# Optimization experiments

Measured on AMD Instinct MI355X. Metric: run time of the kernel, lower is better.

## Reference

```python
import jax, jax.numpy as jnp
import numpy as np

B, S, D, H = 2, 2048, 512, 8
HD = D // H
SPARSITY = 0.15
KTOP = max(1, int(S * SPARSITY))          # 307 important rows
HALF_WIN = min(32, S // 4) // 2           # 16 -> window |i-j| <= 16
RC = min(16, S // 8)                      # 16 random links per query token


def setup_inputs() -> dict:
    key = jax.random.key(0)
    ks = jax.random.split(key, 8)
    s = 0.02
    return {
        "x":  jax.random.normal(ks[0], (B, S, D), jnp.float32),
        "Wq": jax.random.normal(ks[1], (D, D), jnp.float32) * s,
        "bq": jnp.zeros((D,), jnp.float32),
        "Wk": jax.random.normal(ks[2], (D, D), jnp.float32) * s,
        "bk": jnp.zeros((D,), jnp.float32),
        "Wv": jax.random.normal(ks[3], (D, D), jnp.float32) * s,
        "bv": jnp.zeros((D,), jnp.float32),
        "Wo": jax.random.normal(ks[4], (D, D), jnp.float32) * s,
        "bo": jnp.zeros((D,), jnp.float32),
        "Ws1": jax.random.normal(ks[5], (D, D // 2), jnp.float32) * s,
        "bs1": jnp.zeros((D // 2,), jnp.float32),
        "Ws2": jax.random.normal(ks[6], (D // 2, 1), jnp.float32) * s,
        "bs2": jnp.zeros((1,), jnp.float32),
        # models torch.randperm(S)[:RC] per (b, i); duplicates are harmless for set-to-1
        "rand_idx": jax.random.randint(ks[7], (B, S, RC), 0, S, jnp.int32),
    }


def _sparse_mask(x, Ws1, bs1, Ws2, bs2, rand_idx):
    # importance scorer: Linear -> ReLU -> Linear -> Sigmoid, squeeze(-1)
    imp = jax.nn.sigmoid(jax.nn.relu(x @ Ws1 + bs1) @ Ws2 + bs2)[..., 0]  # [B,S]
    _, top_idx = jax.lax.top_k(imp, KTOP)                                  # [B,KTOP]
    brange = jnp.arange(B)
    row_imp = jnp.zeros((B, S), bool).at[brange[:, None], top_idx].set(True)
    idx = jnp.arange(S)
    win = jnp.abs(idx[:, None] - idx[None, :]) <= HALF_WIN                 # [S,S]
    rmask = jnp.zeros((B, S, S), bool).at[
        brange[:, None, None], idx[None, :, None], rand_idx].set(True)    # [B,S,S]
    mask = row_imp[:, :, None] | win[None, :, :] | rmask                   # [B,S,S]
    tril = idx[:, None] >= idx[None, :]                                    # causal (mask * (causal==0))
    return mask & tril


def reference(x, Wq, bq, Wk, bk, Wv, bv, Wo, bo, Ws1, bs1, Ws2, bs2, rand_idx):
    allowed = _sparse_mask(x, Ws1, bs1, Ws2, bs2, rand_idx)                # [B,S,S] bool
    q = (x @ Wq + bq).reshape(B, S, H, HD).transpose(0, 2, 1, 3)           # [B,H,S,HD]
    k = (x @ Wk + bk).reshape(B, S, H, HD).transpose(0, 2, 1, 3)
    v = (x @ Wv + bv).reshape(B, S, H, HD).transpose(0, 2, 1, 3)
    scores = jnp.einsum('bhid,bhjd->bhij', q, k) / jnp.sqrt(jnp.float32(HD))
    scores = jnp.where(allowed[:, None, :, :], scores, -jnp.inf)
    attn = jax.nn.softmax(scores, axis=-1)                                 # every row has j=i allowed
    out = jnp.einsum('bhij,bhjd->bhid', attn, v)
    out = out.transpose(0, 2, 1, 3).reshape(B, S, D)
    return out @ Wo + bo
```

## Files before the change

kernel.cpp:

```cpp
#include <hip/hip_runtime.h>
#include <math.h>

typedef unsigned short u16;
typedef unsigned int u32;
typedef unsigned long long u64;
typedef short bf16x8 __attribute__((ext_vector_type(8)));
typedef float f32x4 __attribute__((ext_vector_type(4)));

constexpr int NB = 2, NS = 2048, ND = 512, NH = 8, NHD = 64;
constexpr int NKTOP = 307, NHWIN = 16, NRC = 16;
constexpr int NILIST = 320;
constexpr int NSPAR = NS - NKTOP;
constexpr int NSPAD = 1744;
constexpr int NCHUNK = 8;
constexpr int LDSPAD = 40;
constexpr int LDSK64 = 72;
constexpr int PSTR = 72;

__device__ __forceinline__ u16 f2bf(float f) {
  u32 u = __builtin_bit_cast(u32, f);
  u32 r = (u + 0x7FFFu + ((u >> 16) & 1u)) >> 16;
  return (u16)r;
}
__device__ __forceinline__ float bf2f(short v) {
  return __builtin_bit_cast(float, (u32)(u16)v << 16);
}

__global__ __launch_bounds__(256) void csa_cvt_w(const float* __restrict__ W0, const float* __restrict__ W1,
                                                 const float* __restrict__ W2, const float* __restrict__ W3,
                                                 u16* __restrict__ wt) {
  __shared__ float tile[64][33];
  int w = blockIdx.z;
  const float* src = (w == 0) ? W0 : (w == 1) ? W1 : (w == 2) ? W2 : W3;
  int kb = blockIdx.x * 64, nb = blockIdx.y * 32;
  int tx = threadIdx.x & 31, ty = threadIdx.x >> 5;
  for (int i = ty; i < 64; i += 8) tile[i][tx] = src[(size_t)(kb + i) * ND + nb + tx];
  __syncthreads();
  u16* dst = wt + (size_t)w * ND * ND;
  for (int n = ty; n < 32; n += 8) {
    u32 pk = (u32)f2bf(tile[2 * tx][n]) | ((u32)f2bf(tile[2 * tx + 1][n]) << 16);
    *(u32*)(&dst[(size_t)(nb + n) * ND + kb + 2 * tx]) = pk;
  }
}

__global__ __launch_bounds__(256) void csa_scorer(const float* __restrict__ x, const float* __restrict__ Ws1,
                                                  const float* __restrict__ bs1, const float* __restrict__ Ws2,
                                                  float* __restrict__ part) {
  __shared__ float As[32][68];
  __shared__ float Bs[32][68];
  const int tid = threadIdx.x;
  const int m0 = blockIdx.x * 64, n0 = blockIdx.y * 64;
  const int ty = tid >> 4, tx = tid & 15;
  float acc[4][4] = {};
  const int arow = tid & 63, aks = (tid >> 6) * 8;
  const int bk = tid >> 3, bc = (tid & 7) * 8;
  for (int k0 = 0; k0 < ND; k0 += 32) {
    __syncthreads();
    {
      float4 a0 = *(const float4*)(&x[(size_t)(m0 + arow) * ND + k0 + aks]);
      float4 a1 = *(const float4*)(&x[(size_t)(m0 + arow) * ND + k0 + aks + 4]);
      As[aks + 0][arow] = a0.x; As[aks + 1][arow] = a0.y;
      As[aks + 2][arow] = a0.z; As[aks + 3][arow] = a0.w;
      As[aks + 4][arow] = a1.x; As[aks + 5][arow] = a1.y;
      As[aks + 6][arow] = a1.z; As[aks + 7][arow] = a1.w;
    }
    *(float4*)(&Bs[bk][bc]) = *(const float4*)(&Ws1[(size_t)(k0 + bk) * 256 + n0 + bc]);
    *(float4*)(&Bs[bk][bc + 4]) = *(const float4*)(&Ws1[(size_t)(k0 + bk) * 256 + n0 + bc + 4]);
    __syncthreads();
    for (int k = 0; k < 32; k++) {
      float4 av = *(const float4*)(&As[k][ty * 4]);
      float4 bv = *(const float4*)(&Bs[k][tx * 4]);
      float aa[4] = {av.x, av.y, av.z, av.w};
      float bb[4] = {bv.x, bv.y, bv.z, bv.w};
      for (int i = 0; i < 4; i++)
        for (int j = 0; j < 4; j++)
          acc[i][j] += aa[i] * bb[j];
    }
  }
  float4 w2 = *(const float4*)(&Ws2[n0 + tx * 4]);
  float4 b1 = *(const float4*)(&bs1[n0 + tx * 4]);
  for (int i = 0; i < 4; i++) {
    float p = fmaxf(acc[i][0] + b1.x, 0.f) * w2.x + fmaxf(acc[i][1] + b1.y, 0.f) * w2.y +
              fmaxf(acc[i][2] + b1.z, 0.f) * w2.z + fmaxf(acc[i][3] + b1.w, 0.f) * w2.w;
    for (int off = 1; off < 16; off <<= 1) p += __shfl_xor(p, off, 64);
    if (tx == 0) part[(size_t)(m0 + ty * 4 + i) * 4 + blockIdx.y] = p;
  }
}

__global__ __launch_bounds__(256) void csa_rank(const float* __restrict__ part, int* __restrict__ rowimp) {
  __shared__ float vals[NS];
  const int b = blockIdx.y;
  {
    int t8 = threadIdx.x * 8;
    for (int e = 0; e < 8; e++) {
      float4 pp = *(const float4*)(&part[(size_t)(b * NS + t8 + e) * 4]);
      vals[t8 + e] = (pp.x + pp.y) + (pp.z + pp.w);
    }
  }
  __syncthreads();
  const int wave = threadIdx.x >> 6, lane = threadIdx.x & 63;
  const int s0 = blockIdx.x * 8 + wave * 2;
  const int s1 = s0 + 1;
  const float v0 = vals[s0], v1 = vals[s1];
  int r0 = 0, r1 = 0;
  for (int t = lane; t < NS; t += 64) {
    float u = vals[t];
    r0 += (int)((u > v0) | ((u == v0) & (t < s0)));
    r1 += (int)((u > v1) | ((u == v1) & (t < s1)));
  }
  for (int off = 1; off < 64; off <<= 1) {
    r0 += __shfl_xor(r0, off, 64);
    r1 += __shfl_xor(r1, off, 64);
  }
  if (lane == 0) {
    rowimp[b * NS + s0] = (r0 < NKTOP) ? 1 : 0;
    rowimp[b * NS + s1] = (r1 < NKTOP) ? 1 : 0;
  }
}

__global__ __launch_bounds__(256) void csa_ilist(const int* __restrict__ rowimp, int* __restrict__ ilist,
                                                 int* __restrict__ nlist) {
  __shared__ int cs[256];
  int b = blockIdx.x, t = threadIdx.x;
  int flags[8], sum = 0;
  for (int k = 0; k < 8; k++) {
    flags[k] = rowimp[b * NS + t * 8 + k];
    sum += flags[k];
  }
  cs[t] = sum;
  __syncthreads();
  for (int off = 1; off < 256; off <<= 1) {
    int v = (t >= off) ? cs[t - off] : 0;
    __syncthreads();
    cs[t] += v;
    __syncthreads();
  }
  int pos = cs[t] - sum;
  for (int k = 0; k < 8; k++) {
    int r = t * 8 + k;
    if (flags[k]) ilist[b * NILIST + pos++] = r;
    else nlist[b * NSPAD + (r - pos)] = r;
  }
  if (t < NILIST - NKTOP) ilist[b * NILIST + NKTOP + t] = -1;
  if (t < NSPAD - NSPAR) nlist[b * NSPAD + NSPAR + t] = -1;
}

__global__ __launch_bounds__(256) void csa_gemm_qkv(const float* __restrict__ x, const u16* __restrict__ Bt,
                                                    const float* __restrict__ bq, const float* __restrict__ bk,
                                                    const float* __restrict__ bv, u16* __restrict__ qb,
                                                    u16* __restrict__ kb, u16* __restrict__ vtb,
                                                    u16* __restrict__ vb) {
  __shared__ __attribute__((aligned(16))) u16 As[128 * LDSPAD];
  __shared__ __attribute__((aligned(16))) u16 Bs[64 * LDSPAD];
  const int tid = threadIdx.x;
  const int wave = tid >> 6, lane = tid & 63;
  const int quad = lane >> 4, col = lane & 15;
  const int m0 = blockIdx.x * 128;
  const int n0 = blockIdx.y * 64;
  const f32x4 zf = {0.f, 0.f, 0.f, 0.f};
  f32x4 acc[2][4] = {{zf, zf, zf, zf}, {zf, zf, zf, zf}};
  const int sar = tid >> 1, sak = (tid & 1) * 16;
  const int sbr = tid >> 2, sbk = (tid & 3) * 8;
  for (int k0 = 0; k0 < ND; k0 += 32) {
    __syncthreads();
    {
      const float* xp = &x[(size_t)(m0 + sar) * ND + k0 + sak];
      float4 v0 = *(const float4*)(xp), v1 = *(const float4*)(xp + 4);
      float4 v2 = *(const float4*)(xp + 8), v3 = *(const float4*)(xp + 12);
      u32 w0 = (u32)f2bf(v0.x) | ((u32)f2bf(v0.y) << 16);
      u32 w1 = (u32)f2bf(v0.z) | ((u32)f2bf(v0.w) << 16);
      u32 w2 = (u32)f2bf(v1.x) | ((u32)f2bf(v1.y) << 16);
      u32 w3 = (u32)f2bf(v1.z) | ((u32)f2bf(v1.w) << 16);
      u32 w4 = (u32)f2bf(v2.x) | ((u32)f2bf(v2.y) << 16);
      u32 w5 = (u32)f2bf(v2.z) | ((u32)f2bf(v2.w) << 16);
      u32 w6 = (u32)f2bf(v3.x) | ((u32)f2bf(v3.y) << 16);
      u32 w7 = (u32)f2bf(v3.z) | ((u32)f2bf(v3.w) << 16);
      u32* ap = (u32*)&As[sar * LDSPAD + sak];
      ap[0] = w0; ap[1] = w1; ap[2] = w2; ap[3] = w3;
      ap[4] = w4; ap[5] = w5; ap[6] = w6; ap[7] = w7;
    }
    *(uint4*)(&Bs[sbr * LDSPAD + sbk]) = *(const uint4*)(&Bt[(size_t)(n0 + sbr) * ND + k0 + sbk]);
    __syncthreads();
    bf16x8 af0 = *(const bf16x8*)(&As[(wave * 32 + col) * LDSPAD + quad * 8]);
    bf16x8 af1 = *(const bf16x8*)(&As[(wave * 32 + 16 + col) * LDSPAD + quad * 8]);
    for (int c = 0; c < 4; c++) {
      bf16x8 bfr = *(const bf16x8*)(&Bs[(c * 16 + col) * LDSPAD + quad * 8]);
      acc[0][c] = __builtin_amdgcn_mfma_f32_16x16x32_bf16(af0, bfr, acc[0][c], 0, 0, 0);
      acc[1][c] = __builtin_amdgcn_mfma_f32_16x16x32_bf16(af1, bfr, acc[1][c], 0, 0, 0);
    }
  }
  const int w = n0 >> 9;
  const float* bias = (w == 0) ? bq : (w == 1) ? bk : bv;
  for (int c = 0; c < 4; c++) {
    const int ng = n0 + c * 16 + col;
    const int nn = ng & 511, hh = nn >> 6, hd = nn & 63;
    const float bvv = bias[nn];
    for (int r = 0; r < 2; r++) {
      for (int rr = 0; rr < 4; rr++) {
        const int m = m0 + wave * 32 + r * 16 + quad * 4 + rr;
        const int bb = m >> 11, s = m & (NS - 1);
        u16 v16 = f2bf(acc[r][c][rr] + bvv);
        if (w == 0) qb[((size_t)(bb * NH + hh) * NS + s) * NHD + hd] = v16;
        else if (w == 1) kb[((size_t)(bb * NH + hh) * NS + s) * NHD + hd] = v16;
        else {
          vtb[((size_t)(bb * NH + hh) * NHD + hd) * NS + s] = v16;
          vb[((size_t)(bb * NH + hh) * NS + s) * NHD + hd] = v16;
        }
      }
    }
  }
}

__global__ __launch_bounds__(256) void csa_gemm_out(const u16* __restrict__ A, const u16* __restrict__ Bt,
                                                    const float* __restrict__ bias, float* __restrict__ outp) {
  __shared__ __attribute__((aligned(16))) u16 As[64 * LDSK64];
  __shared__ __attribute__((aligned(16))) u16 Bs[64 * LDSK64];
  const int tid = threadIdx.x;
  const int wave = tid >> 6, lane = tid & 63;
  const int quad = lane >> 4, col = lane & 15;
  const int m0 = blockIdx.x * 64;
  const int n0 = blockIdx.y * 64;
  const f32x4 zf = {0.f, 0.f, 0.f, 0.f};
  f32x4 acc[4] = {zf, zf, zf, zf};
  const int sr = tid >> 2, sk = (tid & 3) * 16;
  for (int k0 = 0; k0 < ND; k0 += 64) {
    __syncthreads();
    *(uint4*)(&As[sr * LDSK64 + sk]) = *(const uint4*)(&A[(size_t)(m0 + sr) * ND + k0 + sk]);
    *(uint4*)(&As[sr * LDSK64 + sk + 8]) = *(const uint4*)(&A[(size_t)(m0 + sr) * ND + k0 + sk + 8]);
    *(uint4*)(&Bs[sr * LDSK64 + sk]) = *(const uint4*)(&Bt[(size_t)(n0 + sr) * ND + k0 + sk]);
    *(uint4*)(&Bs[sr * LDSK64 + sk + 8]) = *(const uint4*)(&Bt[(size_t)(n0 + sr) * ND + k0 + sk + 8]);
    __syncthreads();
    bf16x8 af0 = *(const bf16x8*)(&As[(wave * 16 + col) * LDSK64 + quad * 8]);
    bf16x8 af1 = *(const bf16x8*)(&As[(wave * 16 + col) * LDSK64 + 32 + quad * 8]);
    for (int nt = 0; nt < 4; nt++) {
      bf16x8 bf0 = *(const bf16x8*)(&Bs[(nt * 16 + col) * LDSK64 + quad * 8]);
      bf16x8 bf1 = *(const bf16x8*)(&Bs[(nt * 16 + col) * LDSK64 + 32 + quad * 8]);
      acc[nt] = __builtin_amdgcn_mfma_f32_16x16x32_bf16(af0, bf0, acc[nt], 0, 0, 0);
      acc[nt] = __builtin_amdgcn_mfma_f32_16x16x32_bf16(af1, bf1, acc[nt], 0, 0, 0);
    }
  }
  for (int nt = 0; nt < 4; nt++) {
    const int n = n0 + nt * 16 + col;
    const float bvv = bias[n];
    for (int r = 0; r < 4; r++) {
      const int m = m0 + wave * 16 + quad * 4 + r;
      outp[(size_t)m * ND + n] = acc[nt][r] + bvv;
    }
  }
}

__global__ __launch_bounds__(64) void csa_attn_imp(const u16* __restrict__ qb, const u16* __restrict__ kb,
                                                   const u16* __restrict__ vtb, const int* __restrict__ ilist,
                                                   float* __restrict__ pbuf) {
  const int lane = threadIdx.x;
  const int quad = lane >> 4, col = lane & 15;
  const int qt = blockIdx.x;
  const int chunk = blockIdx.y;
  const int bh = blockIdx.z;
  const int b = bh >> 3, h = bh & 7;

  const int* il = ilist + b * NILIST;
  const u16* qptr = qb + (size_t)(b * NH + h) * NS * NHD;
  const u16* kptr = kb + (size_t)(b * NH + h) * NS * NHD;
  const u16* vptr = vtb + (size_t)(b * NH + h) * NHD * NS;

  const int iq = il[qt * 16 + col];
  const int qrow = (iq < 0) ? 0 : iq;
  bf16x8 qf0 = *(const bf16x8*)(qptr + qrow * NHD + quad * 8);
  bf16x8 qf1 = *(const bf16x8*)(qptr + qrow * NHD + 32 + quad * 8);

  const f32x4 zf = {0.f, 0.f, 0.f, 0.f};
  float m_r[4], l_r[4];
  f32x4 of[4];
  int irow[4];
  for (int r = 0; r < 4; r++) {
    m_r[r] = -INFINITY;
    l_r[r] = 0.f;
    irow[r] = il[qt * 16 + quad * 4 + r];
  }
  for (int n = 0; n < 4; n++) of[n] = zf;

  __shared__ __attribute__((aligned(16))) u16 Pl[16 * PSTR];

  const int max_i = il[(qt * 16 + 15 > NKTOP - 1) ? (NKTOP - 1) : (qt * 16 + 15)];
  const int ntiles = (max_i >> 6) + 1;
  for (int t = chunk; t < ntiles; t += NCHUNK) {
    const int j0 = t * 64;
    f32x4 cg[4];
    for (int g = 0; g < 4; g++) {
      const int jb = j0 + g * 16;
      bf16x8 k0f = *(const bf16x8*)(kptr + (jb + col) * NHD + quad * 8);
      bf16x8 k1f = *(const bf16x8*)(kptr + (jb + col) * NHD + 32 + quad * 8);
      f32x4 c = zf;
      c = __builtin_amdgcn_mfma_f32_16x16x32_bf16(qf0, k0f, c, 0, 0, 0);
      c = __builtin_amdgcn_mfma_f32_16x16x32_bf16(qf1, k1f, c, 0, 0, 0);
      cg[g] = c;
    }
    float ps[4][4], alpha[4];
    for (int r = 0; r < 4; r++) {
      const int i = irow[r];
      float s[4];
      float vmax = -INFINITY;
      for (int g = 0; g < 4; g++) {
        s[g] = (j0 + g * 16 + col <= i) ? cg[g][r] * 0.125f : -INFINITY;
        vmax = fmaxf(vmax, s[g]);
      }
      for (int off = 1; off < 16; off <<= 1) vmax = fmaxf(vmax, __shfl_xor(vmax, off, 64));
      float newm = fmaxf(m_r[r], vmax);
      bool dead = (newm == -INFINITY);
      float a = dead ? 1.f : __expf(m_r[r] - newm);
      float psum = 0.f;
      for (int g = 0; g < 4; g++) {
        float p = dead ? 0.f : __expf(s[g] - newm);
        ps[r][g] = p;
        psum += p;
      }
      for (int off = 1; off < 16; off <<= 1) psum += __shfl_xor(psum, off, 64);
      m_r[r] = newm;
      l_r[r] = l_r[r] * a + psum;
      alpha[r] = a;
    }
    for (int n = 0; n < 4; n++)
      for (int r = 0; r < 4; r++) of[n][r] *= alpha[r];
    __syncthreads();
    for (int r = 0; r < 4; r++)
      for (int g = 0; g < 4; g++)
        Pl[(quad * 4 + r) * PSTR + g * 16 + col] = f2bf(ps[r][g]);
    __syncthreads();
    bf16x8 pf0 = *(const bf16x8*)(&Pl[col * PSTR + quad * 8]);
    bf16x8 pf1 = *(const bf16x8*)(&Pl[col * PSTR + 32 + quad * 8]);
    for (int vn = 0; vn < 4; vn++) {
      bf16x8 vf0 = *(const bf16x8*)(vptr + (size_t)(vn * 16 + col) * NS + j0 + quad * 8);
      bf16x8 vf1 = *(const bf16x8*)(vptr + (size_t)(vn * 16 + col) * NS + j0 + 32 + quad * 8);
      of[vn] = __builtin_amdgcn_mfma_f32_16x16x32_bf16(pf0, vf0, of[vn], 0, 0, 0);
      of[vn] = __builtin_amdgcn_mfma_f32_16x16x32_bf16(pf1, vf1, of[vn], 0, 0, 0);
    }
  }
  float* pr = pbuf + ((size_t)(bh * NCHUNK + chunk) * NILIST + qt * 16) * 66;
  for (int r = 0; r < 4; r++) {
    const int row = quad * 4 + r;
    if (col == 0) {
      pr[row * 66 + 0] = m_r[r];
      pr[row * 66 + 1] = l_r[r];
    }
    for (int vn = 0; vn < 4; vn++)
      pr[row * 66 + 2 + vn * 16 + col] = of[vn][r];
  }
}

__global__ __launch_bounds__(64) void csa_merge(const float* __restrict__ pbuf, const int* __restrict__ ilist,
                                                u16* __restrict__ attnb) {
  const int kp = blockIdx.x, h = blockIdx.y, b = blockIdx.z;
  const int lane = threadIdx.x;
  const int z = b * NH + h;
  float mc[NCHUNK], lc[NCHUNK], mstar = -INFINITY;
  for (int c = 0; c < NCHUNK; c++) {
    const float* base = pbuf + ((size_t)(z * NCHUNK + c) * NILIST + kp) * 66;
    mc[c] = base[0];
    lc[c] = base[1];
    mstar = fmaxf(mstar, mc[c]);
  }
  float lsum = 0.f, osum = 0.f;
  for (int c = 0; c < NCHUNK; c++) {
    const float* base = pbuf + ((size_t)(z * NCHUNK + c) * NILIST + kp) * 66;
    float w = (mc[c] == -INFINITY) ? 0.f : __expf(mc[c] - mstar);
    lsum += w * lc[c];
    osum += w * base[2 + lane];
  }
  const int i = ilist[b * NILIST + kp];
  attnb[((size_t)(b * NS + i) * NH + h) * NHD + lane] = f2bf(osum / lsum);
}

__global__ __launch_bounds__(256) void csa_attn_sparse(const u16* __restrict__ qb, const u16* __restrict__ kb,
                                                       const u16* __restrict__ vb, const int* __restrict__ nlist,
                                                       const int* __restrict__ rand_idx, u16* __restrict__ attnb) {
  __shared__ __attribute__((aligned(16))) u16 ql[4][64];
  __shared__ float pl[4][33];
  __shared__ int jl[4][33];
  const int wave = threadIdx.x >> 6, lane = threadIdx.x & 63;
  const int slot = blockIdx.x * 4 + wave;
  const int h = blockIdx.y, b = blockIdx.z;
  const int i = nlist[b * NSPAD + slot];
  const int iv = (i < 0) ? 0 : i;

  const u16* qrow = qb + ((size_t)(b * NH + h) * NS + iv) * NHD;
  const u16* kbase = kb + (size_t)(b * NH + h) * NS * NHD;
  const u16* vbase = vb + (size_t)(b * NH + h) * NS * NHD;

  if (lane < 8) *(bf16x8*)(&ql[wave][lane * 8]) = *(const bf16x8*)(qrow + lane * 8);
  __syncthreads();

  float sd = bf2f((short)ql[wave][lane]) * bf2f((short)kbase[(size_t)iv * NHD + lane]);
  for (int off = 1; off < 64; off <<= 1) sd += __shfl_xor(sd, off, 64);
  sd *= 0.125f;

  const int c = lane >> 1, half = lane & 1;
  int j, valid;
  if (c < 16) {
    j = i - NHWIN + c;
    valid = (j >= 0);
  } else {
    const int* rr = rand_idx + ((size_t)b * NS + iv) * NRC;
    const int cr = c - 16;
    j = rr[cr];
    valid = (j <= i - NHWIN - 1);
    for (int cp = 0; cp < cr; cp++) valid &= (rr[cp] != j);
  }
  const int jr = valid ? j : 0;
  float s = 0.f;
  {
    const u16* krow = kbase + (size_t)jr * NHD + half * 32;
    for (int c8 = 0; c8 < 4; c8++) {
      bf16x8 kv = *(const bf16x8*)(krow + c8 * 8);
      bf16x8 qv = *(const bf16x8*)(&ql[wave][half * 32 + c8 * 8]);
      for (int e = 0; e < 8; e++) s += bf2f(qv[e]) * bf2f(kv[e]);
    }
  }
  s += __shfl_xor(s, 1, 64);
  s = valid ? s * 0.125f : -INFINITY;

  float smax = s;
  for (int off = 1; off < 64; off <<= 1) smax = fmaxf(smax, __shfl_xor(smax, off, 64));
  smax = fmaxf(smax, sd);
  float p = valid ? __expf(s - smax) : 0.f;
  float pd = __expf(sd - smax);
  float pm = (half == 0) ? p : 0.f;
  for (int off = 1; off < 64; off <<= 1) pm += __shfl_xor(pm, off, 64);
  const float lsum = pm + pd;

  if (half == 0) {
    pl[wave][c] = p;
    jl[wave][c] = jr;
  }
  if (lane == 0) {
    pl[wave][32] = pd;
    jl[wave][32] = iv;
  }
  __syncthreads();

  float o = 0.f;
  for (int jj = 0; jj < 33; jj++) {
    const int jk = __builtin_amdgcn_readfirstlane(jl[wave][jj]);
    const float pj = pl[wave][jj];
    o += pj * bf2f((short)vbase[(size_t)jk * NHD + lane]);
  }
  if (i >= 0)
    attnb[((size_t)(b * NS + i) * NH + h) * NHD + lane] = f2bf(o / lsum);
}

extern "C" void kernel_launch(void* const* d_in, const int* in_sizes, int n_in,
                              void* d_out, int out_size, void* d_ws, size_t ws_size,
                              hipStream_t stream) {
  const float* x = (const float*)d_in[0];
  const float* bq = (const float*)d_in[2];
  const float* bk = (const float*)d_in[4];
  const float* bv = (const float*)d_in[6];
  const float* bo = (const float*)d_in[8];
  const float* Ws1 = (const float*)d_in[9];
  const float* bs1 = (const float*)d_in[10];
  const float* Ws2 = (const float*)d_in[11];
  const int* rand_idx = (const int*)d_in[13];
  float* out = (float*)d_out;

  char* p = (char*)d_ws;
  u16* wt = (u16*)p;         p += (size_t)4 * ND * ND * 2;
  u16* qbuf = (u16*)p;       p += (size_t)NB * NH * NS * NHD * 2;
  u16* kbuf = (u16*)p;       p += (size_t)NB * NH * NS * NHD * 2;
  u16* vtbuf = (u16*)p;      p += (size_t)NB * NH * NHD * NS * 2;
  u16* vbuf = (u16*)p;       p += (size_t)NB * NH * NS * NHD * 2;
  u16* attnb = (u16*)p;      p += (size_t)NB * NS * ND * 2;
  float* part = (float*)p;   p += (size_t)NB * NS * 4 * 4;
  int* rowimp = (int*)p;     p += (size_t)NB * NS * 4;
  int* ilist = (int*)p;      p += (size_t)NB * NILIST * 4;
  int* nlist = (int*)p;      p += (size_t)NB * NSPAD * 4;
  float* pbuf = (float*)p;

  csa_cvt_w<<<dim3(8, 16, 4), 256, 0, stream>>>((const float*)d_in[1], (const float*)d_in[3],
                                                (const float*)d_in[5], (const float*)d_in[7], wt);

  csa_scorer<<<dim3(NB * NS / 64, 4), 256, 0, stream>>>(x, Ws1, bs1, Ws2, part);
  csa_rank<<<dim3(NS / 8, NB), 256, 0, stream>>>(part, rowimp);
  csa_ilist<<<dim3(NB), 256, 0, stream>>>(rowimp, ilist, nlist);

  csa_gemm_qkv<<<dim3(32, 24), 256, 0, stream>>>(x, wt, bq, bk, bv, qbuf, kbuf, vtbuf, vbuf);

  csa_attn_imp<<<dim3(NILIST / 16, NCHUNK, NB * NH), 64, 0, stream>>>(qbuf, kbuf, vtbuf, ilist, pbuf);
  csa_attn_sparse<<<dim3(NSPAD / 4, NH, NB), 256, 0, stream>>>(qbuf, kbuf, vbuf, nlist, rand_idx, attnb);
  csa_merge<<<dim3(NKTOP, NH, NB), 64, 0, stream>>>(pbuf, ilist, attnb);

  csa_gemm_out<<<dim3(64, 8), 256, 0, stream>>>(attnb, wt + 3 * (size_t)ND * ND, bo, out);
}
```

Before: 209.5 us.

## Merge weight-convert/scorer and sparse/important attention kernels; use wave-local LDS fences

After: 217.7 us. +3.9%, slower.

```diff
diff --git a/kernel.cpp b/kernel.cpp
--- a/kernel.cpp
+++ b/kernel.cpp
@@ -16,6 +16,8 @@
 constexpr int LDSPAD = 40;
 constexpr int LDSK64 = 72;
 constexpr int PSTR = 72;
+constexpr int NSBLK = (NSPAD / 4) * NH * NB;
+constexpr int NIBLK = (NILIST / 16) * NCHUNK * (NB * NH) / 4;
 
 __device__ __forceinline__ u16 f2bf(float f) {
   u32 u = __builtin_bit_cast(u32, f);
@@ -25,65 +27,72 @@
 __device__ __forceinline__ float bf2f(short v) {
   return __builtin_bit_cast(float, (u32)(u16)v << 16);
 }
-
-__global__ __launch_bounds__(256) void csa_cvt_w(const float* __restrict__ W0, const float* __restrict__ W1,
-                                                 const float* __restrict__ W2, const float* __restrict__ W3,
-                                                 u16* __restrict__ wt) {
-  __shared__ float tile[64][33];
-  int w = blockIdx.z;
-  const float* src = (w == 0) ? W0 : (w == 1) ? W1 : (w == 2) ? W2 : W3;
-  int kb = blockIdx.x * 64, nb = blockIdx.y * 32;
-  int tx = threadIdx.x & 31, ty = threadIdx.x >> 5;
-  for (int i = ty; i < 64; i += 8) tile[i][tx] = src[(size_t)(kb + i) * ND + nb + tx];
-  __syncthreads();
-  u16* dst = wt + (size_t)w * ND * ND;
-  for (int n = ty; n < 32; n += 8) {
-    u32 pk = (u32)f2bf(tile[2 * tx][n]) | ((u32)f2bf(tile[2 * tx + 1][n]) << 16);
-    *(u32*)(&dst[(size_t)(nb + n) * ND + kb + 2 * tx]) = pk;
-  }
-}
-
-__global__ __launch_bounds__(256) void csa_scorer(const float* __restrict__ x, const float* __restrict__ Ws1,
-                                                  const float* __restrict__ bs1, const float* __restrict__ Ws2,
-                                                  float* __restrict__ part) {
-  __shared__ float As[32][68];
-  __shared__ float Bs[32][68];
+__device__ __forceinline__ void wave_lds_fence() {
+  __builtin_amdgcn_s_waitcnt(0xC07F);
+  __builtin_amdgcn_wave_barrier();
+}
+
+__global__ __launch_bounds__(256) void csa_prep(const float* __restrict__ W0, const float* __restrict__ W1,
+                                                const float* __restrict__ W2, const float* __restrict__ W3,
+                                                u16* __restrict__ wt, const float* __restrict__ x,
+                                                const float* __restrict__ Ws1, const float* __restrict__ bs1,
+                                                const float* __restrict__ Ws2, float* __restrict__ part) {
+  __shared__ float sh[2 * 32 * 68];
   const int tid = threadIdx.x;
-  const int m0 = blockIdx.x * 64, n0 = blockIdx.y * 64;
-  const int ty = tid >> 4, tx = tid & 15;
-  float acc[4][4] = {};
-  const int arow = tid & 63, aks = (tid >> 6) * 8;
-  const int bk = tid >> 3, bc = (tid & 7) * 8;
-  for (int k0 = 0; k0 < ND; k0 += 32) {
-    __syncthreads();
-    {
-      float4 a0 = *(const float4*)(&x[(size_t)(m0 + arow) * ND + k0 + aks]);
-      float4 a1 = *(const float4*)(&x[(size_t)(m0 + arow) * ND + k0 + aks + 4]);
-      As[aks + 0][arow] = a0.x; As[aks + 1][arow] = a0.y;
-      As[aks + 2][arow] = a0.z; As[aks + 3][arow] = a0.w;
-      As[aks + 4][arow] = a1.x; As[aks + 5][arow] = a1.y;
-      As[aks + 6][arow] = a1.z; As[aks + 7][arow] = a1.w;
-    }
-    *(float4*)(&Bs[bk][bc]) = *(const float4*)(&Ws1[(size_t)(k0 + bk) * 256 + n0 + bc]);
-    *(float4*)(&Bs[bk][bc + 4]) = *(const float4*)(&Ws1[(size_t)(k0 + bk) * 256 + n0 + bc + 4]);
-    __syncthreads();
-    for (int k = 0; k < 32; k++) {
-      float4 av = *(const float4*)(&As[k][ty * 4]);
-      float4 bv = *(const float4*)(&Bs[k][tx * 4]);
-      float aa[4] = {av.x, av.y, av.z, av.w};
-      float bb[4] = {bv.x, bv.y, bv.z, bv.w};
-      for (int i = 0; i < 4; i++)
-        for (int j = 0; j < 4; j++)
-          acc[i][j] += aa[i] * bb[j];
-    }
-  }
-  float4 w2 = *(const float4*)(&Ws2[n0 + tx * 4]);
-  float4 b1 = *(const float4*)(&bs1[n0 + tx * 4]);
-  for (int i = 0; i < 4; i++) {
-    float p = fmaxf(acc[i][0] + b1.x, 0.f) * w2.x + fmaxf(acc[i][1] + b1.y, 0.f) * w2.y +
-              fmaxf(acc[i][2] + b1.z, 0.f) * w2.z + fmaxf(acc[i][3] + b1.w, 0.f) * w2.w;
-    for (int off = 1; off < 16; off <<= 1) p += __shfl_xor(p, off, 64);
-    if (tx == 0) part[(size_t)(m0 + ty * 4 + i) * 4 + blockIdx.y] = p;
+  if (blockIdx.x < 256) {
+    const int m0 = (blockIdx.x & 63) * 64, n0 = (blockIdx.x >> 6) * 64;
+    float(*As)[68] = (float(*)[68])sh;
+    float(*Bs)[68] = (float(*)[68])(sh + 32 * 68);
+    const int ty = tid >> 4, tx = tid & 15;
+    float acc[4][4] = {};
+    const int arow = tid & 63, aks = (tid >> 6) * 8;
+    const int bk = tid >> 3, bc = (tid & 7) * 8;
+    for (int k0 = 0; k0 < ND; k0 += 32) {
+      __syncthreads();
+      {
+        float4 a0 = *(const float4*)(&x[(size_t)(m0 + arow) * ND + k0 + aks]);
+        float4 a1 = *(const float4*)(&x[(size_t)(m0 + arow) * ND + k0 + aks + 4]);
+        As[aks + 0][arow] = a0.x; As[aks + 1][arow] = a0.y;
+        As[aks + 2][arow] = a0.z; As[aks + 3][arow] = a0.w;
+        As[aks + 4][arow] = a1.x; As[aks + 5][arow] = a1.y;
+        As[aks + 6][arow] = a1.z; As[aks + 7][arow] = a1.w;
+      }
+      *(float4*)(&Bs[bk][bc]) = *(const float4*)(&Ws1[(size_t)(k0 + bk) * 256 + n0 + bc]);
+      *(float4*)(&Bs[bk][bc + 4]) = *(const float4*)(&Ws1[(size_t)(k0 + bk) * 256 + n0 + bc + 4]);
+      __syncthreads();
+      for (int k = 0; k < 32; k++) {
+        float4 av = *(const float4*)(&As[k][ty * 4]);
+        float4 bv = *(const float4*)(&Bs[k][tx * 4]);
+        float aa[4] = {av.x, av.y, av.z, av.w};
+        float bb[4] = {bv.x, bv.y, bv.z, bv.w};
+        for (int i = 0; i < 4; i++)
+          for (int j = 0; j < 4; j++)
+            acc[i][j] += aa[i] * bb[j];
+      }
+    }
+    float4 w2 = *(const float4*)(&Ws2[n0 + tx * 4]);
+    float4 b1 = *(const float4*)(&bs1[n0 + tx * 4]);
+    for (int i = 0; i < 4; i++) {
+      float p = fmaxf(acc[i][0] + b1.x, 0.f) * w2.x + fmaxf(acc[i][1] + b1.y, 0.f) * w2.y +
+                fmaxf(acc[i][2] + b1.z, 0.f) * w2.z + fmaxf(acc[i][3] + b1.w, 0.f) * w2.w;
+      for (int off = 1; off < 16; off <<= 1) p += __shfl_xor(p, off, 64);
+      if (tx == 0) part[(size_t)(m0 + ty * 4 + i) * 4 + (blockIdx.x >> 6)] = p;
+    }
+  } else {
+    const int cb = blockIdx.x - 256;
+    const int w = cb >> 7;
+    const int kb = ((cb & 127) >> 4) * 64;
+    const int nb = (cb & 15) * 32;
+    const float* src = (w == 0) ? W0 : (w == 1) ? W1 : (w == 2) ? W2 : W3;
+    float(*tile)[33] = (float(*)[33])sh;
+    int tx = tid & 31, ty = tid >> 5;
+    for (int i = ty; i < 64; i += 8) tile[i][tx] = src[(size_t)(kb + i) * ND + nb + tx];
+    __syncthreads();
+    u16* dst = wt + (size_t)w * ND * ND;
+    for (int n = ty; n < 32; n += 8) {
+      u32 pk = (u32)f2bf(tile[2 * tx][n]) | ((u32)f2bf(tile[2 * tx + 1][n]) << 16);
+      *(u32*)(&dst[(size_t)(nb + n) * ND + kb + 2 * tx]) = pk;
+    }
   }
 }
 
@@ -249,102 +258,182 @@
   }
 }
 
-__global__ __launch_bounds__(64) void csa_attn_imp(const u16* __restrict__ qb, const u16* __restrict__ kb,
-                                                   const u16* __restrict__ vtb, const int* __restrict__ ilist,
-                                                   float* __restrict__ pbuf) {
-  const int lane = threadIdx.x;
-  const int quad = lane >> 4, col = lane & 15;
-  const int qt = blockIdx.x;
-  const int chunk = blockIdx.y;
-  const int bh = blockIdx.z;
-  const int b = bh >> 3, h = bh & 7;
-
-  const int* il = ilist + b * NILIST;
-  const u16* qptr = qb + (size_t)(b * NH + h) * NS * NHD;
-  const u16* kptr = kb + (size_t)(b * NH + h) * NS * NHD;
-  const u16* vptr = vtb + (size_t)(b * NH + h) * NHD * NS;
-
-  const int iq = il[qt * 16 + col];
-  const int qrow = (iq < 0) ? 0 : iq;
-  bf16x8 qf0 = *(const bf16x8*)(qptr + qrow * NHD + quad * 8);
-  bf16x8 qf1 = *(const bf16x8*)(qptr + qrow * NHD + 32 + quad * 8);
-
+__global__ __launch_bounds__(256) void csa_attn(const u16* __restrict__ qb, const u16* __restrict__ kb,
+                                                const u16* __restrict__ vb, const u16* __restrict__ vtb,
+                                                const int* __restrict__ ilist, const int* __restrict__ nlist,
+                                                const int* __restrict__ rand_idx, float* __restrict__ pbuf,
+                                                u16* __restrict__ attnb) {
+  __shared__ __attribute__((aligned(16))) char smem[4 * 16 * PSTR * 2];
+  const int wave = threadIdx.x >> 6, lane = threadIdx.x & 63;
   const f32x4 zf = {0.f, 0.f, 0.f, 0.f};
-  float m_r[4], l_r[4];
-  f32x4 of[4];
-  int irow[4];
-  for (int r = 0; r < 4; r++) {
-    m_r[r] = -INFINITY;
-    l_r[r] = 0.f;
-    irow[r] = il[qt * 16 + quad * 4 + r];
-  }
-  for (int n = 0; n < 4; n++) of[n] = zf;
-
-  __shared__ __attribute__((aligned(16))) u16 Pl[16 * PSTR];
-
-  const int max_i = il[(qt * 16 + 15 > NKTOP - 1) ? (NKTOP - 1) : (qt * 16 + 15)];
-  const int ntiles = (max_i >> 6) + 1;
-  for (int t = chunk; t < ntiles; t += NCHUNK) {
-    const int j0 = t * 64;
-    f32x4 cg[4];
-    for (int g = 0; g < 4; g++) {
-      const int jb = j0 + g * 16;
-      bf16x8 k0f = *(const bf16x8*)(kptr + (jb + col) * NHD + quad * 8);
-      bf16x8 k1f = *(const bf16x8*)(kptr + (jb + col) * NHD + 32 + quad * 8);
-      f32x4 c = zf;
-      c = __builtin_amdgcn_mfma_f32_16x16x32_bf16(qf0, k0f, c, 0, 0, 0);
-      c = __builtin_amdgcn_mfma_f32_16x16x32_bf16(qf1, k1f, c, 0, 0, 0);
-      cg[g] = c;
-    }
-    float ps[4][4], alpha[4];
+
+  if (blockIdx.x < NSBLK) {
+    u16* ql = (u16*)smem + wave * 64;
+    float* pl = (float*)(smem + 512) + wave * 33;
+    int* jl = (int*)(smem + 1040) + wave * 33;
+    const int bx = blockIdx.x % (NSPAD / 4);
+    const int rem = blockIdx.x / (NSPAD / 4);
+    const int h = rem & 7, b = rem >> 3;
+    const int slot = bx * 4 + wave;
+    const int i = nlist[b * NSPAD + slot];
+    const int iv = (i < 0) ? 0 : i;
+
+    const u16* qrow = qb + ((size_t)(b * NH + h) * NS + iv) * NHD;
+    const u16* kbase = kb + (size_t)(b * NH + h) * NS * NHD;
+    const u16* vbase = vb + (size_t)(b * NH + h) * NS * NHD;
+
+    if (lane < 8) *(bf16x8*)(&ql[lane * 8]) = *(const bf16x8*)(qrow + lane * 8);
+    wave_lds_fence();
+
+    float sd = bf2f((short)ql[lane]) * bf2f((short)kbase[(size_t)iv * NHD + lane]);
+    for (int off = 1; off < 64; off <<= 1) sd += __shfl_xor(sd, off, 64);
+    sd *= 0.125f;
+
+    const int c = lane >> 1, half = lane & 1;
+    int j, valid;
+    if (c < 16) {
+      j = i - NHWIN + c;
+      valid = (j >= 0);
+    } else {
+      const int* rr = rand_idx + ((size_t)b * NS + iv) * NRC;
+      const int cr = c - 16;
+      j = rr[cr];
+      valid = (j <= i - NHWIN - 1);
+      for (int cp = 0; cp < cr; cp++) valid &= (rr[cp] != j);
+    }
+    const int jr = valid ? j : 0;
+    float s = 0.f;
+    {
+      const u16* krow = kbase + (size_t)jr * NHD + half * 32;
+      for (int c8 = 0; c8 < 4; c8++) {
+        bf16x8 kv = *(const bf16x8*)(krow + c8 * 8);
+        bf16x8 qv = *(const bf16x8*)(&ql[half * 32 + c8 * 8]);
+        for (int e = 0; e < 8; e++) s += bf2f(qv[e]) * bf2f(kv[e]);
+      }
+    }
+    s += __shfl_xor(s, 1, 64);
+    s = valid ? s * 0.125f : -INFINITY;
+
+    float smax = s;
+    for (int off = 1; off < 64; off <<= 1) smax = fmaxf(smax, __shfl_xor(smax, off, 64));
+    smax = fmaxf(smax, sd);
+    float p = valid ? __expf(s - smax) : 0.f;
+    float pd = __expf(sd - smax);
+    float pm = (half == 0) ? p : 0.f;
+    for (int off = 1; off < 64; off <<= 1) pm += __shfl_xor(pm, off, 64);
+    const float lsum = pm + pd;
+
+    if (half == 0) {
+      pl[c] = p;
+      jl[c] = jr;
+    }
+    if (lane == 0) {
+      pl[32] = pd;
+      jl[32] = iv;
+    }
+    wave_lds_fence();
+
+    float o = 0.f;
+    for (int jj = 0; jj < 33; jj++) {
+      const int jk = __builtin_amdgcn_readfirstlane(jl[jj]);
+      const float pj = pl[jj];
+      o += pj * bf2f((short)vbase[(size_t)jk * NHD + lane]);
+    }
+    if (i >= 0)
+      attnb[((size_t)(b * NS + i) * NH + h) * NHD + lane] = f2bf(o / lsum);
+  } else {
+    u16* Pl = (u16*)smem + wave * 16 * PSTR;
+    const int gw = (blockIdx.x - NSBLK) * 4 + wave;
+    const int qt = gw % (NILIST / 16);
+    const int chunk = (gw / (NILIST / 16)) % NCHUNK;
+    const int bh = gw / ((NILIST / 16) * NCHUNK);
+    const int b = bh >> 3, h = bh & 7;
+    const int quad = lane >> 4, col = lane & 15;
+
+    const int* il = ilist + b * NILIST;
+    const u16* qptr = qb + (size_t)(b * NH + h) * NS * NHD;
+    const u16* kptr = kb + (size_t)(b * NH + h) * NS * NHD;
+    const u16* vptr = vtb + (size_t)(b * NH + h) * NHD * NS;
+
+    const int iq = il[qt * 16 + col];
+    const int qrow = (iq < 0) ? 0 : iq;
+    bf16x8 qf0 = *(const bf16x8*)(qptr + qrow * NHD + quad * 8);
+    bf16x8 qf1 = *(const bf16x8*)(qptr + qrow * NHD + 32 + quad * 8);
+
+    float m_r[4], l_r[4];
+    f32x4 of[4];
+    int irow[4];
     for (int r = 0; r < 4; r++) {
-      const int i = irow[r];
-      float s[4];
-      float vmax = -INFINITY;
+      m_r[r] = -INFINITY;
+      l_r[r] = 0.f;
+      irow[r] = il[qt * 16 + quad * 4 + r];
+    }
+    for (int n = 0; n < 4; n++) of[n] = zf;
+
+    const int max_i = il[(qt * 16 + 15 > NKTOP - 1) ? (NKTOP - 1) : (qt * 16 + 15)];
+    const int ntiles = (max_i >> 6) + 1;
+    for (int t = chunk; t < ntiles; t += NCHUNK) {
+      const int j0 = t * 64;
+      f32x4 cg[4];
       for (int g = 0; g < 4; g++) {
-        s[g] = (j0 + g * 16 + col <= i) ? cg[g][r] * 0.125f : -INFINITY;
-        vmax = fmaxf(vmax, s[g]);
-      }
-      for (int off = 1; off < 16; off <<= 1) vmax = fmaxf(vmax, __shfl_xor(vmax, off, 64));
-      float newm = fmaxf(m_r[r], vmax);
-      bool dead = (newm == -INFINITY);
-      float a = dead ? 1.f : __expf(m_r[r] - newm);
-      float psum = 0.f;
-      for (int g = 0; g < 4; g++) {
-        float p = dead ? 0.f : __expf(s[g] - newm);
-        ps[r][g] = p;
-        psum += p;
-      }
-      for (int off = 1; off < 16; off <<= 1) psum += __shfl_xor(psum, off, 64);
-      m_r[r] = newm;
-      l_r[r] = l_r[r] * a + psum;
-      alpha[r] = a;
-    }
-    for (int n = 0; n < 4; n++)
-      for (int r = 0; r < 4; r++) of[n][r] *= alpha[r];
-    __syncthreads();
-    for (int r = 0; r < 4; r++)
-      for (int g = 0; g < 4; g++)
-        Pl[(quad * 4 + r) * PSTR + g * 16 + col] = f2bf(ps[r][g]);
-    __syncthreads();
-    bf16x8 pf0 = *(const bf16x8*)(&Pl[col * PSTR + quad * 8]);
-    bf16x8 pf1 = *(const bf16x8*)(&Pl[col * PSTR + 32 + quad * 8]);
-    for (int vn = 0; vn < 4; vn++) {
-      bf16x8 vf0 = *(const bf16x8*)(vptr + (size_t)(vn * 16 + col) * NS + j0 + quad * 8);
-      bf16x8 vf1 = *(const bf16x8*)(vptr + (size_t)(vn * 16 + col) * NS + j0 + 32 + quad * 8);
-      of[vn] = __builtin_amdgcn_mfma_f32_16x16x32_bf16(pf0, vf0, of[vn], 0, 0, 0);
-      of[vn] = __builtin_amdgcn_mfma_f32_16x16x32_bf16(pf1, vf1, of[vn], 0, 0, 0);
-    }
-  }
-  float* pr = pbuf + ((size_t)(bh * NCHUNK + chunk) * NILIST + qt * 16) * 66;
-  for (int r = 0; r < 4; r++) {
-    const int row = quad * 4 + r;
-    if (col == 0) {
-      pr[row * 66 + 0] = m_r[r];
-      pr[row * 66 + 1] = l_r[r];
-    }
-    for (int vn = 0; vn < 4; vn++)
-      pr[row * 66 + 2 + vn * 16 + col] = of[vn][r];
+        const int jb = j0 + g * 16;
+        bf16x8 k0f = *(const bf16x8*)(kptr + (jb + col) * NHD + quad * 8);
+        bf16x8 k1f = *(const bf16x8*)(kptr + (jb + col) * NHD + 32 + quad * 8);
+        f32x4 cc = zf;
+        cc = __builtin_amdgcn_mfma_f32_16x16x32_bf16(qf0, k0f, cc, 0, 0, 0);
+        cc = __builtin_amdgcn_mfma_f32_16x16x32_bf16(qf1, k1f, cc, 0, 0, 0);
+        cg[g] = cc;
+      }
+      float ps[4][4], alpha[4];
+      for (int r = 0; r < 4; r++) {
+        const int i = irow[r];
+        float s[4];
+        float vmax = -INFINITY;
+        for (int g = 0; g < 4; g++) {
+          s[g] = (j0 + g * 16 + col <= i) ? cg[g][r] * 0.125f : -INFINITY;
+          vmax = fmaxf(vmax, s[g]);
+        }
+        for (int off = 1; off < 16; off <<= 1) vmax = fmaxf(vmax, __shfl_xor(vmax, off, 64));
+        float newm = fmaxf(m_r[r], vmax);
+        bool dead = (newm == -INFINITY);
+        float a = dead ? 1.f : __expf(m_r[r] - newm);
+        float psum = 0.f;
+        for (int g = 0; g < 4; g++) {
+          float pp = dead ? 0.f : __expf(s[g] - newm);
+          ps[r][g] = pp;
+          psum += pp;
+        }
+        for (int off = 1; off < 16; off <<= 1) psum += __shfl_xor(psum, off, 64);
+        m_r[r] = newm;
+        l_r[r] = l_r[r] * a + psum;
+        alpha[r] = a;
+      }
+      for (int n = 0; n < 4; n++)
+        for (int r = 0; r < 4; r++) of[n][r] *= alpha[r];
+      for (int r = 0; r < 4; r++)
+        for (int g = 0; g < 4; g++)
+          Pl[(quad * 4 + r) * PSTR + g * 16 + col] = f2bf(ps[r][g]);
+      wave_lds_fence();
+      bf16x8 pf0 = *(const bf16x8*)(&Pl[col * PSTR + quad * 8]);
+      bf16x8 pf1 = *(const bf16x8*)(&Pl[col * PSTR + 32 + quad * 8]);
+      wave_lds_fence();
+      for (int vn = 0; vn < 4; vn++) {
+        bf16x8 vf0 = *(const bf16x8*)(vptr + (size_t)(vn * 16 + col) * NS + j0 + quad * 8);
+        bf16x8 vf1 = *(const bf16x8*)(vptr + (size_t)(vn * 16 + col) * NS + j0 + 32 + quad * 8);
+        of[vn] = __builtin_amdgcn_mfma_f32_16x16x32_bf16(pf0, vf0, of[vn], 0, 0, 0);
+        of[vn] = __builtin_amdgcn_mfma_f32_16x16x32_bf16(pf1, vf1, of[vn], 0, 0, 0);
+      }
+    }
+    float* pr = pbuf + ((size_t)(bh * NCHUNK + chunk) * NILIST + qt * 16) * 66;
+    for (int r = 0; r < 4; r++) {
+      const int row = quad * 4 + r;
+      if (col == 0) {
+        pr[row * 66 + 0] = m_r[r];
+        pr[row * 66 + 1] = l_r[r];
+      }
+      for (int vn = 0; vn < 4; vn++)
+        pr[row * 66 + 2 + vn * 16 + col] = of[vn][r];
+    }
   }
 }
 
@@ -369,83 +458,6 @@
   }
   const int i = ilist[b * NILIST + kp];
   attnb[((size_t)(b * NS + i) * NH + h) * NHD + lane] = f2bf(osum / lsum);
-}
-
-__global__ __launch_bounds__(256) void csa_attn_sparse(const u16* __restrict__ qb, const u16* __restrict__ kb,
-                                                       const u16* __restrict__ vb, const int* __restrict__ nlist,
-                                                       const int* __restrict__ rand_idx, u16* __restrict__ attnb) {
-  __shared__ __attribute__((aligned(16))) u16 ql[4][64];
-  __shared__ float pl[4][33];
-  __shared__ int jl[4][33];
-  const int wave = threadIdx.x >> 6, lane = threadIdx.x & 63;
-  const int slot = blockIdx.x * 4 + wave;
-  const int h = blockIdx.y, b = blockIdx.z;
-  const int i = nlist[b * NSPAD + slot];
-  const int iv = (i < 0) ? 0 : i;
-
-  const u16* qrow = qb + ((size_t)(b * NH + h) * NS + iv) * NHD;
-  const u16* kbase = kb + (size_t)(b * NH + h) * NS * NHD;
-  const u16* vbase = vb + (size_t)(b * NH + h) * NS * NHD;
-
-  if (lane < 8) *(bf16x8*)(&ql[wave][lane * 8]) = *(const bf16x8*)(qrow + lane * 8);
-  __syncthreads();
-
-  float sd = bf2f((short)ql[wave][lane]) * bf2f((short)kbase[(size_t)iv * NHD + lane]);
-  for (int off = 1; off < 64; off <<= 1) sd += __shfl_xor(sd, off, 64);
-  sd *= 0.125f;
-
-  const int c = lane >> 1, half = lane & 1;
-  int j, valid;
-  if (c < 16) {
-    j = i - NHWIN + c;
-    valid = (j >= 0);
-  } else {
-    const int* rr = rand_idx + ((size_t)b * NS + iv) * NRC;
-    const int cr = c - 16;
-    j = rr[cr];
-    valid = (j <= i - NHWIN - 1);
-    for (int cp = 0; cp < cr; cp++) valid &= (rr[cp] != j);
-  }
-  const int jr = valid ? j : 0;
-  float s = 0.f;
-  {
-    const u16* krow = kbase + (size_t)jr * NHD + half * 32;
-    for (int c8 = 0; c8 < 4; c8++) {
-      bf16x8 kv = *(const bf16x8*)(krow + c8 * 8);
-      bf16x8 qv = *(const bf16x8*)(&ql[wave][half * 32 + c8 * 8]);
-      for (int e = 0; e < 8; e++) s += bf2f(qv[e]) * bf2f(kv[e]);
-    }
-  }
-  s += __shfl_xor(s, 1, 64);
-  s = valid ? s * 0.125f : -INFINITY;
-
-  float smax = s;
-  for (int off = 1; off < 64; off <<= 1) smax = fmaxf(smax, __shfl_xor(smax, off, 64));
-  smax = fmaxf(smax, sd);
-  float p = valid ? __expf(s - smax) : 0.f;
-  float pd = __expf(sd - smax);
-  float pm = (half == 0) ? p : 0.f;
-  for (int off = 1; off < 64; off <<= 1) pm += __shfl_xor(pm, off, 64);
-  const float lsum = pm + pd;
-
-  if (half == 0) {
-    pl[wave][c] = p;
-    jl[wave][c] = jr;
-  }
-  if (lane == 0) {
-    pl[wave][32] = pd;
-    jl[wave][32] = iv;
-  }
-  __syncthreads();
-
-  float o = 0.f;
-  for (int jj = 0; jj < 33; jj++) {
-    const int jk = __builtin_amdgcn_readfirstlane(jl[wave][jj]);
-    const float pj = pl[wave][jj];
-    o += pj * bf2f((short)vbase[(size_t)jk * NHD + lane]);
-  }
-  if (i >= 0)
-    attnb[((size_t)(b * NS + i) * NH + h) * NHD + lane] = f2bf(o / lsum);
 }
 
 extern "C" void kernel_launch(void* const* d_in, const int* in_sizes, int n_in,
@@ -475,17 +487,16 @@
   int* nlist = (int*)p;      p += (size_t)NB * NSPAD * 4;
   float* pbuf = (float*)p;
 
-  csa_cvt_w<<<dim3(8, 16, 4), 256, 0, stream>>>((const float*)d_in[1], (const float*)d_in[3],
-                                                (const float*)d_in[5], (const float*)d_in[7], wt);
-
-  csa_scorer<<<dim3(NB * NS / 64, 4), 256, 0, stream>>>(x, Ws1, bs1, Ws2, part);
+  csa_prep<<<dim3(768), 256, 0, stream>>>((const float*)d_in[1], (const float*)d_in[3],
+                                          (const float*)d_in[5], (const float*)d_in[7], wt,
+                                          x, Ws1, bs1, Ws2, part);
   csa_rank<<<dim3(NS / 8, NB), 256, 0, stream>>>(part, rowimp);
   csa_ilist<<<dim3(NB), 256, 0, stream>>>(rowimp, ilist, nlist);
 
   csa_gemm_qkv<<<dim3(32, 24), 256, 0, stream>>>(x, wt, bq, bk, bv, qbuf, kbuf, vtbuf, vbuf);
 
-  csa_attn_imp<<<dim3(NILIST / 16, NCHUNK, NB * NH), 64, 0, stream>>>(qbuf, kbuf, vtbuf, ilist, pbuf);
-  csa_attn_sparse<<<dim3(NSPAD / 4, NH, NB), 256, 0, stream>>>(qbuf, kbuf, vbuf, nlist, rand_idx, attnb);
+  csa_attn<<<dim3(NSBLK + NIBLK), 256, 0, stream>>>(qbuf, kbuf, vbuf, vtbuf, ilist, nlist,
+                                                    rand_idx, pbuf, attnb);
   csa_merge<<<dim3(NKTOP, NH, NB), 64, 0, stream>>>(pbuf, ilist, attnb);
 
   csa_gemm_out<<<dim3(64, 8), 256, 0, stream>>>(attnb, wt + 3 * (size_t)ND * ND, bo, out);
```
